# Kernel tuning notes

Measured on AMD Instinct MI355X. Metric: run time of the kernel, lower is better.

Reference implementation:

```python
import jax, jax.numpy as jnp
import numpy as np


def _pool2(t):
    # 2x2 max-pool + 2x2 avg-pool, summed. t: [B, C, H, W] with even H, W
    B, C, H, W = t.shape
    r = t.reshape(B, C, H // 2, 2, W // 2, 2)
    return r.max(axis=(3, 5)) + r.mean(axis=(3, 5))


def setup_inputs() -> dict:
    key = jax.random.key(0)
    k1, k2, k3, k4 = jax.random.split(key, 4)
    B, C, H, W = 32, 256, 56, 56
    x = jax.random.normal(k1, (B, C, H, W), dtype=jnp.float32)
    W1 = jax.random.normal(k2, (C // 2, C), dtype=jnp.float32) * 0.05
    W2 = jax.random.normal(k3, (C // 2, C), dtype=jnp.float32) * 0.05
    W3 = jax.random.normal(k4, (C, C), dtype=jnp.float32) * 0.05
    gamma = jnp.zeros((1,), dtype=jnp.float32)
    return {"x": x, "W1": W1, "W2": W2, "W3": W3, "gamma": gamma}


def reference(x, W1, W2, W3, gamma):
    B, C, H, W = x.shape
    # 1x1 convs (bias-free) == channel matmuls
    c1 = jnp.einsum('oc,bchw->bohw', W1, x)  # [B, C/2, H, W]
    c2 = jnp.einsum('oc,bchw->bohw', W2, x)  # [B, C/2, H, W]
    c3 = jnp.einsum('oc,bchw->bohw', W3, x)  # [B, C,   H, W]
    c1p = _pool2(c1)  # [B, C/2, H/2, W/2]
    c3p = _pool2(c3)  # [B, C,   H/2, W/2]
    n = H * W
    m = n // 4
    c1p_f = c1p.reshape(B, C // 2, m)
    c2_f = c2.reshape(B, C // 2, n)
    c3p_f = c3p.reshape(B, C, m)
    # matrix[b, n, m] = sum_c c2[b,c,n] * c1p[b,c,m]
    matrix = jnp.einsum('bcn,bcm->bnm', c2_f, c1p_f)
    attention = jax.nn.softmax(matrix, axis=-1)  # [B, n, m]
    # refined[b, c, n] = sum_m c3p[b,c,m] * attention[b,n,m]
    refined = jnp.einsum('bcm,bnm->bcn', c3p_f, attention).reshape(B, C, H, W)
    return gamma[0] * refined + x
```

## Files before the change

kernel.cpp:

```cpp
#include <hip/hip_runtime.h>

#define BATCH 32
#define CIN   256
#define CHALF 128
#define NPIX  3136
#define MPOOL 784
#define MPAD  896

typedef __bf16 bf16;
typedef __bf16 bf16x2 __attribute__((ext_vector_type(2)));
typedef __bf16 bf16x4 __attribute__((ext_vector_type(4)));
typedef __bf16 bf16x8 __attribute__((ext_vector_type(8)));
typedef float  f32x4  __attribute__((ext_vector_type(4)));

__global__ __launch_bounds__(256) void k_cast(
    const float* __restrict__ W1, const float* __restrict__ W2,
    const float* __restrict__ W3, bf16* __restrict__ WcatF)
{
    int u = blockIdx.x * 256 + threadIdx.x;
    int lane = u & 63, frag = u >> 6;
    int ks = frag & 7, ot = frag >> 3;
    int o = ot * 16 + (lane & 15);
    int c0 = ks * 32 + (lane >> 4) * 8;
    const float* src = (o < 128) ? (W1 + o * 256)
                     : (o < 256) ? (W2 + (o - 128) * 256)
                                 : (W3 + (o - 256) * 256);
    float4 v0 = *(const float4*)(src + c0);
    float4 v1 = *(const float4*)(src + c0 + 4);
    bf16x8 w = { (bf16)v0.x, (bf16)v0.y, (bf16)v0.z, (bf16)v0.w,
                 (bf16)v1.x, (bf16)v1.y, (bf16)v1.z, (bf16)v1.w };
    *(bf16x8*)(WcatF + (size_t)u * 8) = w;
}

#define XS_STRIDE   528
#define SLAB_STRIDE 520

__global__ __launch_bounds__(512) void k_conv(
    const float* __restrict__ x, const bf16* __restrict__ WcatF,
    bf16* __restrict__ c2n, bf16* __restrict__ c1pT, bf16* __restrict__ c3p)
{
    const int h2 = blockIdx.x, b = blockIdx.y;
    const int t = threadIdx.x;
    const int lane = t & 63, wave = t >> 6;
    const int l15 = lane & 15, lg = lane >> 4;

    __shared__ __align__(16) unsigned char smem[59136];

    if (h2 == 0) {
        float4 z = {0.f, 0.f, 0.f, 0.f};
        float4* p1 = (float4*)(c1pT + (size_t)b * MPAD * CHALF + (size_t)MPOOL * CHALF);
        for (int u = t; u < 1792; u += 512) p1[u] = z;
        bf16* p3 = c3p + (size_t)b * CIN * MPAD + MPOOL;
        for (int u = t; u < 256 * 14; u += 512) {
            int c = u / 14, g = u % 14;
            *(float4*)((char*)(p3 + (size_t)c * MPAD) + g * 16) = z;
        }
    }

    {
        const float* xb = x + (size_t)b * CIN * NPIX + h2 * 112;
        float vv[14][4];
        #pragma unroll
        for (int i = 0; i < 14; ++i) {
            int u = t + i * 512;
            int c4 = u / 112, n = u - c4 * 112;
            const float* s = xb + (size_t)(c4 * 4) * NPIX + n;
            vv[i][0] = s[0];
            vv[i][1] = s[NPIX];
            vv[i][2] = s[2 * NPIX];
            vv[i][3] = s[3 * NPIX];
        }
        #pragma unroll
        for (int i = 0; i < 14; ++i) {
            int u = t + i * 512;
            int c4 = u / 112, n = u - c4 * 112;
            bf16x4 w = {(bf16)vv[i][0], (bf16)vv[i][1], (bf16)vv[i][2], (bf16)vv[i][3]};
            *(bf16x4*)(smem + n * XS_STRIDE + c4 * 8) = w;
        }
    }
    __syncthreads();

    f32x4 acc[4][7];
    #pragma unroll
    for (int fo = 0; fo < 4; ++fo)
        #pragma unroll
        for (int fn = 0; fn < 7; ++fn) {
            f32x4 zz = {0.f, 0.f, 0.f, 0.f};
            acc[fo][fn] = zz;
        }
    {
        const unsigned char* xsb = smem + l15 * XS_STRIDE + lg * 16;
        const bf16* wfb = WcatF + (((size_t)wave * 4) * 8 + 0) * 64 * 8 + (size_t)lane * 8;
        #pragma unroll
        for (int ks = 0; ks < 8; ++ks) {
            bf16x8 afr[4], bfr[7];
            #pragma unroll
            for (int fo = 0; fo < 4; ++fo)
                afr[fo] = *(const bf16x8*)(wfb + (size_t)(fo * 8 + ks) * 64 * 8);
            #pragma unroll
            for (int fn = 0; fn < 7; ++fn)
                bfr[fn] = *(const bf16x8*)(xsb + fn * 16 * XS_STRIDE + ks * 64);
            #pragma unroll
            for (int fo = 0; fo < 4; ++fo)
                #pragma unroll
                for (int fn = 0; fn < 7; ++fn)
                    acc[fo][fn] = __builtin_amdgcn_mfma_f32_16x16x32_bf16(
                        afr[fo], bfr[fn], acc[fo][fn], 0, 0, 0);
        }
    }

    __syncthreads();
    if (wave < 4) {
        #pragma unroll
        for (int fo = 0; fo < 4; ++fo)
            #pragma unroll
            for (int fn = 0; fn < 7; ++fn) {
                int n = fn * 16 + l15;
                int ol = wave * 64 + fo * 16 + lg * 4;
                f32x4 a = acc[fo][fn];
                bf16x4 w = {(bf16)a[0], (bf16)a[1], (bf16)a[2], (bf16)a[3]};
                *(bf16x4*)(smem + n * SLAB_STRIDE + ol * 2) = w;
            }
    }
    __syncthreads();
    {
        bf16* dst = c1pT + (size_t)b * MPAD * CHALF + (size_t)h2 * 28 * CHALF;
        for (int u = t; u < 896; u += 512) {
            int w2 = u >> 5, o4 = (u & 31) * 4;
            bf16x4 r0 = *(bf16x4*)(smem + (2 * w2)      * SLAB_STRIDE + o4 * 2);
            bf16x4 r1 = *(bf16x4*)(smem + (2 * w2 + 1)  * SLAB_STRIDE + o4 * 2);
            bf16x4 r2 = *(bf16x4*)(smem + (56 + 2 * w2) * SLAB_STRIDE + o4 * 2);
            bf16x4 r3 = *(bf16x4*)(smem + (57 + 2 * w2) * SLAB_STRIDE + o4 * 2);
            bf16x4 o_;
            #pragma unroll
            for (int j = 0; j < 4; ++j) {
                float p0 = (float)r0[j], p1 = (float)r1[j];
                float p2 = (float)r2[j], p3 = (float)r3[j];
                float mx = fmaxf(fmaxf(p0, p1), fmaxf(p2, p3));
                float av = (p0 + p1 + p2 + p3) * 0.25f;
                o_[j] = (bf16)(mx + av);
            }
            *(bf16x4*)(dst + (size_t)w2 * CHALF + o4) = o_;
        }
    }
    {
        bf16* dst = c2n + (size_t)b * NPIX * CHALF + (size_t)h2 * 112 * CHALF;
        for (int u = t; u < 3584; u += 512) {
            int n = u >> 5, o4 = (u & 31) * 4;
            bf16x4 v = *(bf16x4*)(smem + n * SLAB_STRIDE + 256 + o4 * 2);
            *(bf16x4*)(dst + (size_t)n * CHALF + o4) = v;
        }
    }

    __syncthreads();
    if (wave >= 4) {
        #pragma unroll
        for (int fo = 0; fo < 4; ++fo)
            #pragma unroll
            for (int fn = 0; fn < 7; ++fn) {
                int n = fn * 16 + l15;
                int ol = (wave - 4) * 64 + fo * 16 + lg * 4;
                f32x4 a = acc[fo][fn];
                bf16x4 w = {(bf16)a[0], (bf16)a[1], (bf16)a[2], (bf16)a[3]};
                *(bf16x4*)(smem + n * SLAB_STRIDE + ol * 2) = w;
            }
    }
    __syncthreads();
    {
        bf16* dst = c3p + (size_t)b * CIN * MPAD + h2 * 28;
        for (int u = t; u < 3584; u += 512) {
            int c = u / 14, w2p = u - c * 14;
            bf16x2 o_;
            #pragma unroll
            for (int k = 0; k < 2; ++k) {
                int w2 = 2 * w2p + k;
                float p0 = (float)*(bf16*)(smem + (2 * w2)      * SLAB_STRIDE + c * 2);
                float p1 = (float)*(bf16*)(smem + (2 * w2 + 1)  * SLAB_STRIDE + c * 2);
                float p2 = (float)*(bf16*)(smem + (56 + 2 * w2) * SLAB_STRIDE + c * 2);
                float p3 = (float)*(bf16*)(smem + (57 + 2 * w2) * SLAB_STRIDE + c * 2);
                float mx = fmaxf(fmaxf(p0, p1), fmaxf(p2, p3));
                float av = (p0 + p1 + p2 + p3) * 0.25f;
                o_[k] = (bf16)(mx + av);
            }
            *(bf16x2*)(dst + (size_t)c * MPAD + 2 * w2p) = o_;
        }
    }
}

#define STG_OFF 114688

__global__ __launch_bounds__(512) void k_attn(
    const bf16* __restrict__ c2n,
    const bf16* __restrict__ c1pT,
    const bf16* __restrict__ c3p,
    const float* __restrict__ x,
    const float* __restrict__ gamma,
    float* __restrict__ out)
{
    const int nb = blockIdx.x, b = blockIdx.y;
    const int n0 = nb * 64;
    const int t = threadIdx.x;
    const int lane = t & 63, wave = t >> 6;
    const int l15 = lane & 15, lg = lane >> 4;
    const int p = wave & 3, h = wave >> 2;

    __shared__ __align__(16) unsigned char smem[147456];
    unsigned char* stg = smem + STG_OFF;
    float* EX = (float*)stg;

    bf16x8 bq[4];
    {
        const bf16* c2b = c2n + ((size_t)b * NPIX + n0 + p * 16 + l15) * CHALF + lg * 8;
        #pragma unroll
        for (int k = 0; k < 4; ++k) bq[k] = *(const bf16x8*)(c2b + k * 32);
    }
    const bf16* c1b = c1pT + (size_t)b * MPAD * CHALF;
    const bf16* c3b = c3p + (size_t)b * CIN * MPAD;

    const int r0 = t >> 4, s0 = t & 15;
    const int cs = (s0 & 8) | ((s0 & 7) ^ (r0 & 7));
    const bf16* sA = c1b + (size_t)r0 * CHALF + cs * 8;
    const bf16* sB = c1b + (size_t)(448 + r0) * CHALF + cs * 8;

    uint4 rXa, rXb, rYa, rYb;
    rXa = *(const uint4*)(sA);
    rXb = *(const uint4*)(sB);
    *(uint4*)(stg + t * 16) = rXa;
    *(uint4*)(stg + 8192 + t * 16) = rXb;
    rYa = *(const uint4*)(sA + 4096);
    rYb = *(const uint4*)(sB + 4096);
    __syncthreads();

    f32x4 sacc[28];
    #pragma unroll
    for (int j = 0; j < 28; ++j) {
        f32x4 z = {0.f, 0.f, 0.f, 0.f};
        sacc[j] = z;
    }

    #pragma unroll
    for (int mc = 0; mc < 14; ++mc) {
        const unsigned char* bufc = stg + (mc & 1) * 16384;
        unsigned char* bufn = stg + ((mc & 1) ^ 1) * 16384;
        if (mc + 1 < 14) {
            if (mc & 1) { *(uint4*)(bufn + t * 16) = rXa; *(uint4*)(bufn + 8192 + t * 16) = rXb; }
            else        { *(uint4*)(bufn + t * 16) = rYa; *(uint4*)(bufn + 8192 + t * 16) = rYb; }
        }
        if (mc + 2 < 14) {
            if (mc & 1) { rYa = *(const uint4*)(sA + (mc + 2) * 4096); rYb = *(const uint4*)(sB + (mc + 2) * 4096); }
            else        { rXa = *(const uint4*)(sA + (mc + 2) * 4096); rXb = *(const uint4*)(sB + (mc + 2) * 4096); }
        }
        #pragma unroll
        for (int sf = 0; sf < 2; ++sf) {
            bf16x8 af[4];
            #pragma unroll
            for (int k = 0; k < 4; ++k)
                af[k] = *(const bf16x8*)(bufc + h * 8192 + (sf * 16 + l15) * 256
                                         + ((lg * 16 + k * 64) ^ ((l15 & 7) << 4)));
            #pragma unroll
            for (int k = 0; k < 4; ++k)
                sacc[mc * 2 + sf] = __builtin_amdgcn_mfma_f32_16x16x32_bf16(
                    af[k], bq[k], sacc[mc * 2 + sf], 0, 0, 0);
        }
        __syncthreads();
    }

    float mx = -1e30f;
    #pragma unroll
    for (int j = 0; j < 28; ++j) {
        if (h == 0 || j < 21)
            mx = fmaxf(mx, fmaxf(fmaxf(sacc[j][0], sacc[j][1]),
                                 fmaxf(sacc[j][2], sacc[j][3])));
    }
    mx = fmaxf(mx, __shfl_xor(mx, 16));
    mx = fmaxf(mx, __shfl_xor(mx, 32));
    if (lane < 16) EX[wave * 16 + l15] = mx;
    __syncthreads();
    mx = fmaxf(mx, EX[(wave ^ 4) * 16 + l15]);

    float s = 0.f;
    #pragma unroll
    for (int j = 0; j < 28; ++j) {
        if (h == 0 || j < 21) {
            #pragma unroll
            for (int r = 0; r < 4; ++r) {
                float e = __expf(sacc[j][r] - mx);
                sacc[j][r] = e;
                s += e;
            }
        }
    }
    s += __shfl_xor(s, 16);
    s += __shfl_xor(s, 32);
    if (lane < 16) EX[128 + wave * 16 + l15] = s;
    __syncthreads();
    s += EX[128 + (wave ^ 4) * 16 + l15];
    const float ri = 1.f / s;

    const int pc = t >> 2, ps = t & 3;
    const bf16* sV  = c3b + (size_t)pc * MPAD + ((ps ^ ((pc >> 1) & 3)) * 8);
    const bf16* sV2 = c3b + (size_t)(pc + 128) * MPAD + ((ps ^ ((pc >> 1) & 3)) * 8);
    rXa = *(const uint4*)(sV);
    rXb = *(const uint4*)(sV2);

    {
        const int n = p * 16 + l15;
        const unsigned sw = (unsigned)((n & 7) << 4);
        const unsigned rowb = (unsigned)(n * 1792);
        #pragma unroll
        for (int j = 0; j < 28; ++j) {
            bf16x4 w;
            if (h == 0 || j < 21) {
                w = bf16x4{ (bf16)(sacc[j][0] * ri), (bf16)(sacc[j][1] * ri),
                            (bf16)(sacc[j][2] * ri), (bf16)(sacc[j][3] * ri) };
            } else {
                w = bf16x4{ (bf16)0.f, (bf16)0.f, (bf16)0.f, (bf16)0.f };
            }
            unsigned byte = rowb + (unsigned)(h * 896 + j * 32 + lg * 8);
            *(bf16x4*)(smem + (byte ^ sw)) = w;
        }
    }
    __syncthreads();

    *(uint4*)(stg + t * 16) = rXa;
    *(uint4*)(stg + 8192 + t * 16) = rXb;
    rYa = *(const uint4*)(sV + 32);
    rYb = *(const uint4*)(sV2 + 32);
    __syncthreads();

    const int wn = h, wq = p;
    f32x4 acc2[2][4];
    #pragma unroll
    for (int fn = 0; fn < 2; ++fn)
        #pragma unroll
        for (int fc = 0; fc < 4; ++fc) {
            f32x4 z = {0.f, 0.f, 0.f, 0.f};
            acc2[fn][fc] = z;
        }

    #pragma unroll
    for (int ks = 0; ks < 28; ++ks) {
        const unsigned char* bufc = stg + (ks & 1) * 16384;
        unsigned char* bufn = stg + ((ks & 1) ^ 1) * 16384;
        if (ks + 1 < 28) {
            if (ks & 1) { *(uint4*)(bufn + t * 16) = rXa; *(uint4*)(bufn + 8192 + t * 16) = rXb; }
            else        { *(uint4*)(bufn + t * 16) = rYa; *(uint4*)(bufn + 8192 + t * 16) = rYb; }
        }
        if (ks + 2 < 28) {
            if (ks & 1) { rYa = *(const uint4*)(sV + (ks + 2) * 32); rYb = *(const uint4*)(sV2 + (ks + 2) * 32); }
            else        { rXa = *(const uint4*)(sV + (ks + 2) * 32); rXb = *(const uint4*)(sV2 + (ks + 2) * 32); }
        }
        {
            int nA0 = wn * 32 + l15, nA1 = nA0 + 16;
            int mb = (ks * 32 + lg * 8) * 2;
            bf16x8 af0 = *(const bf16x8*)(smem + ((nA0 * 1792 + mb) ^ ((nA0 & 7) << 4)));
            bf16x8 af1 = *(const bf16x8*)(smem + ((nA1 * 1792 + mb) ^ ((nA1 & 7) << 4)));
            #pragma unroll
            for (int fc = 0; fc < 4; ++fc) {
                int c = wq * 64 + fc * 16 + l15;
                bf16x8 bfr = *(const bf16x8*)(bufc + c * 64 + ((lg ^ ((c >> 1) & 3)) * 16));
                acc2[0][fc] = __builtin_amdgcn_mfma_f32_16x16x32_bf16(af0, bfr, acc2[0][fc], 0, 0, 0);
                acc2[1][fc] = __builtin_amdgcn_mfma_f32_16x16x32_bf16(af1, bfr, acc2[1][fc], 0, 0, 0);
            }
        }
        __syncthreads();
    }

    float* R = (float*)smem;
    #pragma unroll
    for (int fn = 0; fn < 2; ++fn)
        #pragma unroll
        for (int fc = 0; fc < 4; ++fc) {
            int c = wq * 64 + fc * 16 + l15;
            #pragma unroll
            for (int r = 0; r < 4; ++r) {
                int n = wn * 32 + fn * 16 + lg * 4 + r;
                R[n * 257 + c] = acc2[fn][fc][r];
            }
        }
    __syncthreads();
    const float g = gamma[0];
    const float* xb = x + (size_t)b * CIN * NPIX + n0;
    float* ob = out + (size_t)b * CIN * NPIX + n0;
    #pragma unroll 4
    for (int i = 0; i < 32; ++i) {
        int idx = t + i * 512;
        int c = idx >> 6, nn = idx & 63;
        size_t off = (size_t)c * NPIX + nn;
        ob[off] = g * R[nn * 257 + c] + xb[off];
    }
}

extern "C" void kernel_launch(void* const* d_in, const int* in_sizes, int n_in,
                              void* d_out, int out_size, void* d_ws, size_t ws_size,
                              hipStream_t stream) {
    const float* x     = (const float*)d_in[0];
    const float* W1    = (const float*)d_in[1];
    const float* W2    = (const float*)d_in[2];
    const float* W3    = (const float*)d_in[3];
    const float* gamma = (const float*)d_in[4];
    float* out = (float*)d_out;

    bf16* ws    = (bf16*)d_ws;
    bf16* WcatF = ws;
    bf16* c2n   = WcatF + (size_t)512 * 256;
    bf16* c1pT  = c2n + (size_t)BATCH * NPIX * CHALF;
    bf16* c3p   = c1pT + (size_t)BATCH * MPAD * CHALF;

    k_cast<<<64, 256, 0, stream>>>(W1, W2, W3, WcatF);
    k_conv<<<dim3(28, BATCH), 512, 0, stream>>>(x, WcatF, c2n, c1pT, c3p);
    k_attn<<<dim3(49, BATCH), 512, 0, stream>>>(c2n, c1pT, c3p, x, gamma, out);
}
```

Baseline: 239.8 us.

## Store pooled K/V in MFMA fragment order and load fragments directly from global

```diff
diff --git a/kernel.cpp b/kernel.cpp
--- a/kernel.cpp
+++ b/kernel.cpp
@@ -12,6 +12,9 @@
 typedef __bf16 bf16x4 __attribute__((ext_vector_type(4)));
 typedef __bf16 bf16x8 __attribute__((ext_vector_type(8)));
 typedef float  f32x4  __attribute__((ext_vector_type(4)));
+
+#define C1PF_B 114688
+#define C3PF_B 229376
 
 __global__ __launch_bounds__(256) void k_cast(
     const float* __restrict__ W1, const float* __restrict__ W2,
@@ -37,7 +40,7 @@
 
 __global__ __launch_bounds__(512) void k_conv(
     const float* __restrict__ x, const bf16* __restrict__ WcatF,
-    bf16* __restrict__ c2n, bf16* __restrict__ c1pT, bf16* __restrict__ c3p)
+    bf16* __restrict__ c2n, bf16* __restrict__ c1pF, bf16* __restrict__ c3pF)
 {
     const int h2 = blockIdx.x, b = blockIdx.y;
     const int t = threadIdx.x;
@@ -47,13 +50,17 @@
     __shared__ __align__(16) unsigned char smem[59136];
 
     if (h2 == 0) {
-        float4 z = {0.f, 0.f, 0.f, 0.f};
-        float4* p1 = (float4*)(c1pT + (size_t)b * MPAD * CHALF + (size_t)MPOOL * CHALF);
-        for (int u = t; u < 1792; u += 512) p1[u] = z;
-        bf16* p3 = c3p + (size_t)b * CIN * MPAD + MPOOL;
-        for (int u = t; u < 256 * 14; u += 512) {
-            int c = u / 14, g = u % 14;
-            *(float4*)((char*)(p3 + (size_t)c * MPAD) + g * 16) = z;
+        float4 z4 = {0.f, 0.f, 0.f, 0.f};
+        float4* p1 = (float4*)(c1pF + (size_t)b * C1PF_B + 100352);
+        for (int u = t; u < 1792; u += 512) p1[u] = z4;
+        bf16* p3 = c3pF + (size_t)b * C3PF_B;
+        bf16x2 z2 = {(bf16)0.f, (bf16)0.f};
+        for (int u = t; u < 14336; u += 512) {
+            int c = u / 56, mp2 = u % 56;
+            int m0 = 784 + 2 * mp2;
+            int ks = m0 >> 5, lgm = (m0 >> 3) & 3, e = m0 & 7;
+            int cf = c >> 4, l15c = c & 15;
+            *(bf16x2*)(p3 + ((((size_t)cf * 28 + ks) * 64) + lgm * 16 + l15c) * 8 + e) = z2;
         }
     }
 
@@ -124,23 +131,27 @@
     }
     __syncthreads();
     {
-        bf16* dst = c1pT + (size_t)b * MPAD * CHALF + (size_t)h2 * 28 * CHALF;
-        for (int u = t; u < 896; u += 512) {
-            int w2 = u >> 5, o4 = (u & 31) * 4;
-            bf16x4 r0 = *(bf16x4*)(smem + (2 * w2)      * SLAB_STRIDE + o4 * 2);
-            bf16x4 r1 = *(bf16x4*)(smem + (2 * w2 + 1)  * SLAB_STRIDE + o4 * 2);
-            bf16x4 r2 = *(bf16x4*)(smem + (56 + 2 * w2) * SLAB_STRIDE + o4 * 2);
-            bf16x4 r3 = *(bf16x4*)(smem + (57 + 2 * w2) * SLAB_STRIDE + o4 * 2);
-            bf16x4 o_;
-            #pragma unroll
-            for (int j = 0; j < 4; ++j) {
+        bf16* dst = c1pF + (size_t)b * C1PF_B;
+        if (t < 448) {
+            int m_local = t >> 4, kl = t & 15;
+            int k = kl >> 2, lg2 = kl & 3;
+            int m = h2 * 28 + m_local;
+            int mf = m >> 4, l15m = m & 15;
+            int cb = (k * 32 + lg2 * 8) * 2;
+            bf16x8 r0 = *(bf16x8*)(smem + (2 * m_local)      * SLAB_STRIDE + cb);
+            bf16x8 r1 = *(bf16x8*)(smem + (2 * m_local + 1)  * SLAB_STRIDE + cb);
+            bf16x8 r2 = *(bf16x8*)(smem + (56 + 2 * m_local) * SLAB_STRIDE + cb);
+            bf16x8 r3 = *(bf16x8*)(smem + (57 + 2 * m_local) * SLAB_STRIDE + cb);
+            bf16x8 o_;
+            #pragma unroll
+            for (int j = 0; j < 8; ++j) {
                 float p0 = (float)r0[j], p1 = (float)r1[j];
                 float p2 = (float)r2[j], p3 = (float)r3[j];
                 float mx = fmaxf(fmaxf(p0, p1), fmaxf(p2, p3));
                 float av = (p0 + p1 + p2 + p3) * 0.25f;
                 o_[j] = (bf16)(mx + av);
             }
-            *(bf16x4*)(dst + (size_t)w2 * CHALF + o4) = o_;
+            *(bf16x8*)(dst + (((size_t)mf * 4 + k) * 64 + lg2 * 16 + l15m) * 8) = o_;
         }
     }
     {
@@ -167,7 +178,7 @@
     }
     __syncthreads();
     {
-        bf16* dst = c3p + (size_t)b * CIN * MPAD + h2 * 28;
+        bf16* dst = c3pF + (size_t)b * C3PF_B;
         for (int u = t; u < 3584; u += 512) {
             int c = u / 14, w2p = u - c * 14;
             bf16x2 o_;
@@ -182,17 +193,18 @@
                 float av = (p0 + p1 + p2 + p3) * 0.25f;
                 o_[k] = (bf16)(mx + av);
             }
-            *(bf16x2*)(dst + (size_t)c * MPAD + 2 * w2p) = o_;
+            int m0 = h2 * 28 + 2 * w2p;
+            int ks = m0 >> 5, lgm = (m0 >> 3) & 3, e = m0 & 7;
+            int cf = c >> 4, l15c = c & 15;
+            *(bf16x2*)(dst + ((((size_t)cf * 28 + ks) * 64) + lgm * 16 + l15c) * 8 + e) = o_;
         }
     }
 }
-
-#define STG_OFF 114688
 
 __global__ __launch_bounds__(512) void k_attn(
     const bf16* __restrict__ c2n,
-    const bf16* __restrict__ c1pT,
-    const bf16* __restrict__ c3p,
+    const bf16* __restrict__ c1pF,
+    const bf16* __restrict__ c3pF,
     const float* __restrict__ x,
     const float* __restrict__ gamma,
     float* __restrict__ out)
@@ -204,9 +216,8 @@
     const int l15 = lane & 15, lg = lane >> 4;
     const int p = wave & 3, h = wave >> 2;
 
-    __shared__ __align__(16) unsigned char smem[147456];
-    unsigned char* stg = smem + STG_OFF;
-    float* EX = (float*)stg;
+    __shared__ __align__(16) unsigned char smem[115712];
+    float* EX = (float*)(smem + 114688);
 
     bf16x8 bq[4];
     {
@@ -214,22 +225,6 @@
         #pragma unroll
         for (int k = 0; k < 4; ++k) bq[k] = *(const bf16x8*)(c2b + k * 32);
     }
-    const bf16* c1b = c1pT + (size_t)b * MPAD * CHALF;
-    const bf16* c3b = c3p + (size_t)b * CIN * MPAD;
-
-    const int r0 = t >> 4, s0 = t & 15;
-    const int cs = (s0 & 8) | ((s0 & 7) ^ (r0 & 7));
-    const bf16* sA = c1b + (size_t)r0 * CHALF + cs * 8;
-    const bf16* sB = c1b + (size_t)(448 + r0) * CHALF + cs * 8;
-
-    uint4 rXa, rXb, rYa, rYb;
-    rXa = *(const uint4*)(sA);
-    rXb = *(const uint4*)(sB);
-    *(uint4*)(stg + t * 16) = rXa;
-    *(uint4*)(stg + 8192 + t * 16) = rXb;
-    rYa = *(const uint4*)(sA + 4096);
-    rYb = *(const uint4*)(sB + 4096);
-    __syncthreads();
 
     f32x4 sacc[28];
     #pragma unroll
@@ -237,32 +232,19 @@
         f32x4 z = {0.f, 0.f, 0.f, 0.f};
         sacc[j] = z;
     }
-
-    #pragma unroll
-    for (int mc = 0; mc < 14; ++mc) {
-        const unsigned char* bufc = stg + (mc & 1) * 16384;
-        unsigned char* bufn = stg + ((mc & 1) ^ 1) * 16384;
-        if (mc + 1 < 14) {
-            if (mc & 1) { *(uint4*)(bufn + t * 16) = rXa; *(uint4*)(bufn + 8192 + t * 16) = rXb; }
-            else        { *(uint4*)(bufn + t * 16) = rYa; *(uint4*)(bufn + 8192 + t * 16) = rYb; }
-        }
-        if (mc + 2 < 14) {
-            if (mc & 1) { rYa = *(const uint4*)(sA + (mc + 2) * 4096); rYb = *(const uint4*)(sB + (mc + 2) * 4096); }
-            else        { rXa = *(const uint4*)(sA + (mc + 2) * 4096); rXb = *(const uint4*)(sB + (mc + 2) * 4096); }
-        }
-        #pragma unroll
-        for (int sf = 0; sf < 2; ++sf) {
+    {
+        const bf16* aF = c1pF + (size_t)b * C1PF_B
+                       + (size_t)(h * 28) * 2048 + (size_t)lane * 8;
+        #pragma unroll
+        for (int j = 0; j < 28; ++j) {
             bf16x8 af[4];
             #pragma unroll
             for (int k = 0; k < 4; ++k)
-                af[k] = *(const bf16x8*)(bufc + h * 8192 + (sf * 16 + l15) * 256
-                                         + ((lg * 16 + k * 64) ^ ((l15 & 7) << 4)));
+                af[k] = *(const bf16x8*)(aF + (size_t)(j * 4 + k) * 512);
             #pragma unroll
             for (int k = 0; k < 4; ++k)
-                sacc[mc * 2 + sf] = __builtin_amdgcn_mfma_f32_16x16x32_bf16(
-                    af[k], bq[k], sacc[mc * 2 + sf], 0, 0, 0);
-        }
-        __syncthreads();
+                sacc[j] = __builtin_amdgcn_mfma_f32_16x16x32_bf16(af[k], bq[k], sacc[j], 0, 0, 0);
+        }
     }
 
     float mx = -1e30f;
@@ -296,12 +278,6 @@
     __syncthreads();
     s += EX[128 + (wave ^ 4) * 16 + l15];
     const float ri = 1.f / s;
-
-    const int pc = t >> 2, ps = t & 3;
-    const bf16* sV  = c3b + (size_t)pc * MPAD + ((ps ^ ((pc >> 1) & 3)) * 8);
-    const bf16* sV2 = c3b + (size_t)(pc + 128) * MPAD + ((ps ^ ((pc >> 1) & 3)) * 8);
-    rXa = *(const uint4*)(sV);
-    rXb = *(const uint4*)(sV2);
 
     {
         const int n = p * 16 + l15;
@@ -322,12 +298,6 @@
     }
     __syncthreads();
 
-    *(uint4*)(stg + t * 16) = rXa;
-    *(uint4*)(stg + 8192 + t * 16) = rXb;
-    rYa = *(const uint4*)(sV + 32);
-    rYb = *(const uint4*)(sV2 + 32);
-    __syncthreads();
-
     const int wn = h, wq = p;
     f32x4 acc2[2][4];
     #pragma unroll
@@ -337,35 +307,27 @@
             f32x4 z = {0.f, 0.f, 0.f, 0.f};
             acc2[fn][fc] = z;
         }
-
-    #pragma unroll
-    for (int ks = 0; ks < 28; ++ks) {
-        const unsigned char* bufc = stg + (ks & 1) * 16384;
-        unsigned char* bufn = stg + ((ks & 1) ^ 1) * 16384;
-        if (ks + 1 < 28) {
-            if (ks & 1) { *(uint4*)(bufn + t * 16) = rXa; *(uint4*)(bufn + 8192 + t * 16) = rXb; }
-            else        { *(uint4*)(bufn + t * 16) = rYa; *(uint4*)(bufn + 8192 + t * 16) = rYb; }
-        }
-        if (ks + 2 < 28) {
-            if (ks & 1) { rYa = *(const uint4*)(sV + (ks + 2) * 32); rYb = *(const uint4*)(sV2 + (ks + 2) * 32); }
-            else        { rXa = *(const uint4*)(sV + (ks + 2) * 32); rXb = *(const uint4*)(sV2 + (ks + 2) * 32); }
-        }
-        {
-            int nA0 = wn * 32 + l15, nA1 = nA0 + 16;
-            int mb = (ks * 32 + lg * 8) * 2;
-            bf16x8 af0 = *(const bf16x8*)(smem + ((nA0 * 1792 + mb) ^ ((nA0 & 7) << 4)));
-            bf16x8 af1 = *(const bf16x8*)(smem + ((nA1 * 1792 + mb) ^ ((nA1 & 7) << 4)));
+    {
+        const bf16* vF = c3pF + (size_t)b * C3PF_B
+                       + (size_t)(wq * 4) * (28 * 512) + (size_t)lane * 8;
+        const int nA0 = wn * 32 + l15, nA1 = nA0 + 16;
+        const unsigned swA0 = (unsigned)((nA0 & 7) << 4), swA1 = (unsigned)((nA1 & 7) << 4);
+        const unsigned rbA0 = (unsigned)(nA0 * 1792), rbA1 = (unsigned)(nA1 * 1792);
+        #pragma unroll
+        for (int ks = 0; ks < 28; ++ks) {
+            unsigned mb = (unsigned)((ks * 32 + lg * 8) * 2);
+            bf16x8 af0 = *(const bf16x8*)(smem + ((rbA0 + mb) ^ swA0));
+            bf16x8 af1 = *(const bf16x8*)(smem + ((rbA1 + mb) ^ swA1));
             #pragma unroll
             for (int fc = 0; fc < 4; ++fc) {
-                int c = wq * 64 + fc * 16 + l15;
-                bf16x8 bfr = *(const bf16x8*)(bufc + c * 64 + ((lg ^ ((c >> 1) & 3)) * 16));
+                bf16x8 bfr = *(const bf16x8*)(vF + (size_t)(fc * 28 + ks) * 512);
                 acc2[0][fc] = __builtin_amdgcn_mfma_f32_16x16x32_bf16(af0, bfr, acc2[0][fc], 0, 0, 0);
                 acc2[1][fc] = __builtin_amdgcn_mfma_f32_16x16x32_bf16(af1, bfr, acc2[1][fc], 0, 0, 0);
             }
         }
-        __syncthreads();
-    }
-
+    }
+
+    __syncthreads();
     float* R = (float*)smem;
     #pragma unroll
     for (int fn = 0; fn < 2; ++fn)
@@ -404,10 +366,10 @@
     bf16* ws    = (bf16*)d_ws;
     bf16* WcatF = ws;
     bf16* c2n   = WcatF + (size_t)512 * 256;
-    bf16* c1pT  = c2n + (size_t)BATCH * NPIX * CHALF;
-    bf16* c3p   = c1pT + (size_t)BATCH * MPAD * CHALF;
+    bf16* c1pF  = c2n + (size_t)BATCH * NPIX * CHALF;
+    bf16* c3pF  = c1pF + (size_t)BATCH * C1PF_B;
 
     k_cast<<<64, 256, 0, stream>>>(W1, W2, W3, WcatF);
-    k_conv<<<dim3(28, BATCH), 512, 0, stream>>>(x, WcatF, c2n, c1pT, c3p);
-    k_attn<<<dim3(49, BATCH), 512, 0, stream>>>(c2n, c1pT, c3p, x, gamma, out);
+    k_conv<<<dim3(28, BATCH), 512, 0, stream>>>(x, WcatF, c2n, c1pF, c3pF);
+    k_attn<<<dim3(49, BATCH), 512, 0, stream>>>(c2n, c1pF, c3pF, x, gamma, out);
 }
```

Measured after the change: 260.0 us. +8.4%, slower.

## Store pooled c3p in MFMA fragment layout and load B operands directly from global

Applied to the files above, without the earlier changes.

```diff
diff --git a/kernel.cpp b/kernel.cpp
--- a/kernel.cpp
+++ b/kernel.cpp
@@ -12,6 +12,8 @@
 typedef __bf16 bf16x4 __attribute__((ext_vector_type(4)));
 typedef __bf16 bf16x8 __attribute__((ext_vector_type(8)));
 typedef float  f32x4  __attribute__((ext_vector_type(4)));
+
+#define C3PF_B 229376
 
 __global__ __launch_bounds__(256) void k_cast(
     const float* __restrict__ W1, const float* __restrict__ W2,
@@ -37,7 +39,7 @@
 
 __global__ __launch_bounds__(512) void k_conv(
     const float* __restrict__ x, const bf16* __restrict__ WcatF,
-    bf16* __restrict__ c2n, bf16* __restrict__ c1pT, bf16* __restrict__ c3p)
+    bf16* __restrict__ c2n, bf16* __restrict__ c1pT, bf16* __restrict__ c3pF)
 {
     const int h2 = blockIdx.x, b = blockIdx.y;
     const int t = threadIdx.x;
@@ -47,13 +49,17 @@
     __shared__ __align__(16) unsigned char smem[59136];
 
     if (h2 == 0) {
-        float4 z = {0.f, 0.f, 0.f, 0.f};
+        float4 z4 = {0.f, 0.f, 0.f, 0.f};
         float4* p1 = (float4*)(c1pT + (size_t)b * MPAD * CHALF + (size_t)MPOOL * CHALF);
-        for (int u = t; u < 1792; u += 512) p1[u] = z;
-        bf16* p3 = c3p + (size_t)b * CIN * MPAD + MPOOL;
-        for (int u = t; u < 256 * 14; u += 512) {
-            int c = u / 14, g = u % 14;
-            *(float4*)((char*)(p3 + (size_t)c * MPAD) + g * 16) = z;
+        for (int u = t; u < 1792; u += 512) p1[u] = z4;
+        bf16* p3 = c3pF + (size_t)b * C3PF_B;
+        bf16x2 z2 = {(bf16)0.f, (bf16)0.f};
+        for (int u = t; u < 14336; u += 512) {
+            int c = u / 56, mp2 = u % 56;
+            int m0 = 784 + 2 * mp2;
+            int ks = m0 >> 5, lgm = (m0 >> 3) & 3, e = m0 & 7;
+            int cf = c >> 4, l15c = c & 15;
+            *(bf16x2*)(p3 + ((((size_t)cf * 28 + ks) * 64) + lgm * 16 + l15c) * 8 + e) = z2;
         }
     }
 
@@ -167,7 +173,7 @@
     }
     __syncthreads();
     {
-        bf16* dst = c3p + (size_t)b * CIN * MPAD + h2 * 28;
+        bf16* dst = c3pF + (size_t)b * C3PF_B;
         for (int u = t; u < 3584; u += 512) {
             int c = u / 14, w2p = u - c * 14;
             bf16x2 o_;
@@ -182,7 +188,10 @@
                 float av = (p0 + p1 + p2 + p3) * 0.25f;
                 o_[k] = (bf16)(mx + av);
             }
-            *(bf16x2*)(dst + (size_t)c * MPAD + 2 * w2p) = o_;
+            int m0 = h2 * 28 + 2 * w2p;
+            int ks = m0 >> 5, lgm = (m0 >> 3) & 3, e = m0 & 7;
+            int cf = c >> 4, l15c = c & 15;
+            *(bf16x2*)(dst + ((((size_t)cf * 28 + ks) * 64) + lgm * 16 + l15c) * 8 + e) = o_;
         }
     }
 }
@@ -192,7 +201,7 @@
 __global__ __launch_bounds__(512) void k_attn(
     const bf16* __restrict__ c2n,
     const bf16* __restrict__ c1pT,
-    const bf16* __restrict__ c3p,
+    const bf16* __restrict__ c3pF,
     const float* __restrict__ x,
     const float* __restrict__ gamma,
     float* __restrict__ out)
@@ -215,7 +224,6 @@
         for (int k = 0; k < 4; ++k) bq[k] = *(const bf16x8*)(c2b + k * 32);
     }
     const bf16* c1b = c1pT + (size_t)b * MPAD * CHALF;
-    const bf16* c3b = c3p + (size_t)b * CIN * MPAD;
 
     const int r0 = t >> 4, s0 = t & 15;
     const int cs = (s0 & 8) | ((s0 & 7) ^ (r0 & 7));
@@ -297,12 +305,6 @@
     s += EX[128 + (wave ^ 4) * 16 + l15];
     const float ri = 1.f / s;
 
-    const int pc = t >> 2, ps = t & 3;
-    const bf16* sV  = c3b + (size_t)pc * MPAD + ((ps ^ ((pc >> 1) & 3)) * 8);
-    const bf16* sV2 = c3b + (size_t)(pc + 128) * MPAD + ((ps ^ ((pc >> 1) & 3)) * 8);
-    rXa = *(const uint4*)(sV);
-    rXb = *(const uint4*)(sV2);
-
     {
         const int n = p * 16 + l15;
         const unsigned sw = (unsigned)((n & 7) << 4);
@@ -322,12 +324,6 @@
     }
     __syncthreads();
 
-    *(uint4*)(stg + t * 16) = rXa;
-    *(uint4*)(stg + 8192 + t * 16) = rXb;
-    rYa = *(const uint4*)(sV + 32);
-    rYb = *(const uint4*)(sV2 + 32);
-    __syncthreads();
-
     const int wn = h, wq = p;
     f32x4 acc2[2][4];
     #pragma unroll
@@ -337,35 +333,27 @@
             f32x4 z = {0.f, 0.f, 0.f, 0.f};
             acc2[fn][fc] = z;
         }
-
-    #pragma unroll
-    for (int ks = 0; ks < 28; ++ks) {
-        const unsigned char* bufc = stg + (ks & 1) * 16384;
-        unsigned char* bufn = stg + ((ks & 1) ^ 1) * 16384;
-        if (ks + 1 < 28) {
-            if (ks & 1) { *(uint4*)(bufn + t * 16) = rXa; *(uint4*)(bufn + 8192 + t * 16) = rXb; }
-            else        { *(uint4*)(bufn + t * 16) = rYa; *(uint4*)(bufn + 8192 + t * 16) = rYb; }
-        }
-        if (ks + 2 < 28) {
-            if (ks & 1) { rYa = *(const uint4*)(sV + (ks + 2) * 32); rYb = *(const uint4*)(sV2 + (ks + 2) * 32); }
-            else        { rXa = *(const uint4*)(sV + (ks + 2) * 32); rXb = *(const uint4*)(sV2 + (ks + 2) * 32); }
-        }
-        {
-            int nA0 = wn * 32 + l15, nA1 = nA0 + 16;
-            int mb = (ks * 32 + lg * 8) * 2;
-            bf16x8 af0 = *(const bf16x8*)(smem + ((nA0 * 1792 + mb) ^ ((nA0 & 7) << 4)));
-            bf16x8 af1 = *(const bf16x8*)(smem + ((nA1 * 1792 + mb) ^ ((nA1 & 7) << 4)));
+    {
+        const bf16* vF = c3pF + (size_t)b * C3PF_B
+                       + (size_t)(wq * 4) * (28 * 512) + (size_t)lane * 8;
+        const int nA0 = wn * 32 + l15, nA1 = nA0 + 16;
+        const unsigned swA0 = (unsigned)((nA0 & 7) << 4), swA1 = (unsigned)((nA1 & 7) << 4);
+        const unsigned rbA0 = (unsigned)(nA0 * 1792), rbA1 = (unsigned)(nA1 * 1792);
+        #pragma unroll
+        for (int ks = 0; ks < 28; ++ks) {
+            unsigned mb = (unsigned)((ks * 32 + lg * 8) * 2);
+            bf16x8 af0 = *(const bf16x8*)(smem + ((rbA0 + mb) ^ swA0));
+            bf16x8 af1 = *(const bf16x8*)(smem + ((rbA1 + mb) ^ swA1));
             #pragma unroll
             for (int fc = 0; fc < 4; ++fc) {
-                int c = wq * 64 + fc * 16 + l15;
-                bf16x8 bfr = *(const bf16x8*)(bufc + c * 64 + ((lg ^ ((c >> 1) & 3)) * 16));
+                bf16x8 bfr = *(const bf16x8*)(vF + (size_t)(fc * 28 + ks) * 512);
                 acc2[0][fc] = __builtin_amdgcn_mfma_f32_16x16x32_bf16(af0, bfr, acc2[0][fc], 0, 0, 0);
                 acc2[1][fc] = __builtin_amdgcn_mfma_f32_16x16x32_bf16(af1, bfr, acc2[1][fc], 0, 0, 0);
             }
         }
-        __syncthreads();
-    }
-
+    }
+
+    __syncthreads();
     float* R = (float*)smem;
     #pragma unroll
     for (int fn = 0; fn < 2; ++fn)
@@ -405,9 +393,9 @@
     bf16* WcatF = ws;
     bf16* c2n   = WcatF + (size_t)512 * 256;
     bf16* c1pT  = c2n + (size_t)BATCH * NPIX * CHALF;
-    bf16* c3p   = c1pT + (size_t)BATCH * MPAD * CHALF;
+    bf16* c3pF  = c1pT + (size_t)BATCH * MPAD * CHALF;
 
     k_cast<<<64, 256, 0, stream>>>(W1, W2, W3, WcatF);
-    k_conv<<<dim3(28, BATCH), 512, 0, stream>>>(x, WcatF, c2n, c1pT, c3p);
-    k_attn<<<dim3(49, BATCH), 512, 0, stream>>>(c2n, c1pT, c3p, x, gamma, out);
+    k_conv<<<dim3(28, BATCH), 512, 0, stream>>>(x, WcatF, c2n, c1pT, c3pF);
+    k_attn<<<dim3(49, BATCH), 512, 0, stream>>>(c2n, c1pT, c3pF, x, gamma, out);
 }
```

After: 253.8 us. +5.9%, slower.
